# Kernel tuning notes

Measured on AMD Instinct MI355X. Metric: run time of the kernel, lower is better.

Reference implementation:

```python
import jax, jax.numpy as jnp
import numpy as np

SOFT_TAU = 0.5
MAX_TEMP = 40.0
LABEL_SMOOTH = 0.1


def setup_inputs() -> dict:
    key = jax.random.key(0)
    k1, k2 = jax.random.split(key)
    B, Tv, Tw, D = 64, 128, 128, 256
    video_features = jax.random.normal(k1, (B, Tv, D), dtype=jnp.float32)
    wifi_features = jax.random.normal(k2, (B, Tw, D), dtype=jnp.float32)
    logit_scale = jnp.ones((), dtype=jnp.float32)
    return {"video_features": video_features, "wifi_features": wifi_features, "logit_scale": logit_scale}


def _cross_entropy_ls(logits, labels):
    # torch CrossEntropyLoss(label_smoothing=0.1), mean reduction
    logp = jax.nn.log_softmax(logits, axis=-1)
    nll = -jnp.take_along_axis(logp, labels[:, None], axis=1)[:, 0]
    smooth = -jnp.mean(logp, axis=-1)
    return jnp.mean((1.0 - LABEL_SMOOTH) * nll + LABEL_SMOOTH * smooth)


def reference(video_features, wifi_features, logit_scale):
    B = video_features.shape[0]
    # [B, B, Tv, Tw] dense cross-modal similarity
    sim = jnp.einsum('imd,jnd->ijmn', video_features, wifi_features)
    sim_d = jax.lax.stop_gradient(sim)
    # video->wifi soft pooling over Tw
    attn_v2w = jax.nn.softmax(sim_d / SOFT_TAU, axis=3)
    soft_sim_v2w = jnp.sum(sim * attn_v2w, axis=3)  # [B, B, Tv]
    # wifi->video soft pooling over Tv
    attn_w2v = jax.nn.softmax(sim_d / SOFT_TAU, axis=2)
    soft_sim_w2v = jnp.sum(sim * attn_w2v, axis=2)  # [B, B, Tw]
    # frame-level softmax pooling to global similarity
    fw_v = jax.nn.softmax(jax.lax.stop_gradient(soft_sim_v2w) / SOFT_TAU, axis=2)
    sim_v2w_global = jnp.sum(soft_sim_v2w * fw_v, axis=2)  # [B, B]
    fw_w = jax.nn.softmax(jax.lax.stop_gradient(soft_sim_w2v) / SOFT_TAU, axis=2)
    sim_w2v_global = jnp.sum(soft_sim_w2v * fw_w, axis=2)  # [B, B]
    dense_similarity = (sim_v2w_global + sim_w2v_global) / 2.0
    scale = jnp.minimum(logit_scale, MAX_TEMP)
    logits_per_video = scale * dense_similarity
    logits_per_wifi = logits_per_video.T
    labels = jnp.arange(B, dtype=jnp.int32)
    loss_video = _cross_entropy_ls(logits_per_video, labels)
    loss_wifi = _cross_entropy_ls(logits_per_wifi, labels)
    return (loss_video + loss_wifi) / 2.0
```

## Files before the change

kernel.cpp:

```cpp
#include <hip/hip_runtime.h>
#include <hip/hip_bf16.h>

typedef __attribute__((ext_vector_type(8))) short bf16x8;
typedef __attribute__((ext_vector_type(4))) float f32x4;

#define TT 128
#define DD 256
#define BK 64
#define BPAN 16384

__device__ __forceinline__ unsigned short f2bf(float f) {
  unsigned int x = __float_as_uint(f);
  x += 0x7fffu + ((x >> 16) & 1u);
  return (unsigned short)(x >> 16);
}

__device__ __forceinline__ bf16x8 pack8(float4 lo, float4 hi) {
  bf16x8 v;
  v[0] = (short)f2bf(lo.x); v[1] = (short)f2bf(lo.y);
  v[2] = (short)f2bf(lo.z); v[3] = (short)f2bf(lo.w);
  v[4] = (short)f2bf(hi.x); v[5] = (short)f2bf(hi.y);
  v[6] = (short)f2bf(hi.z); v[7] = (short)f2bf(hi.w);
  return v;
}

__global__ __launch_bounds__(512, 4) void pair_kernel(
    const float* __restrict__ video, const float* __restrict__ wifi,
    float* __restrict__ dense) {
  __shared__ __align__(16) char lds[65536];
  const int tid = threadIdx.x;
  const int bid = blockIdx.x;
  const int bi = bid >> 6, bj = bid & 63;
  const float* __restrict__ Ag = video + (size_t)bi * (TT * DD);
  const float* __restrict__ Bg = wifi  + (size_t)bj * (TT * DD);

  const int wid = tid >> 6, l = tid & 63;
  const int l15 = l & 15;
  const int R   = (wid >> 1) * 32;
  const int Cc  = (wid & 1) * 64;
  const int xr  = (l15 & 7) << 4;
  const int lhi16 = (l >> 4) * 16;

  const int srow  = tid >> 2;
  const int scolb = (tid & 3) * 32;
  const int sswz  = (srow & 7) << 4;
  const int sb0 = srow * 128 + ((scolb)      ^ sswz);
  const int sb1 = srow * 128 + ((scolb + 16) ^ sswz);

  f32x4 acc[2][4];
#pragma unroll
  for (int m = 0; m < 2; ++m)
#pragma unroll
    for (int n = 0; n < 4; ++n) acc[m][n] = (f32x4){0.f, 0.f, 0.f, 0.f};

  const int arow0 = (R + l15) * 128;
  const int arow1 = (R + 16 + l15) * 128;
  const int brow0 = (Cc +  0 + l15) * 128 + BPAN;
  const int brow1 = (Cc + 16 + l15) * 128 + BPAN;
  const int brow2 = (Cc + 32 + l15) * 128 + BPAN;
  const int brow3 = (Cc + 48 + l15) * 128 + BPAN;

  for (int kp = 0; kp < 4; ++kp) {
    const float* pa = Ag + srow * DD + kp * BK + (tid & 3) * 16;
    const float* pb = Bg + srow * DD + kp * BK + (tid & 3) * 16;
    float4 a0 = *(const float4*)(pa);
    float4 a1 = *(const float4*)(pa + 4);
    float4 a2 = *(const float4*)(pa + 8);
    float4 a3 = *(const float4*)(pa + 12);
    float4 b0 = *(const float4*)(pb);
    float4 b1 = *(const float4*)(pb + 4);
    float4 b2 = *(const float4*)(pb + 8);
    float4 b3 = *(const float4*)(pb + 12);
    if (kp) __syncthreads();
    *(bf16x8*)(lds + sb0)        = pack8(a0, a1);
    *(bf16x8*)(lds + sb1)        = pack8(a2, a3);
    *(bf16x8*)(lds + BPAN + sb0) = pack8(b0, b1);
    *(bf16x8*)(lds + BPAN + sb1) = pack8(b2, b3);
    __syncthreads();

#pragma unroll
    for (int ks = 0; ks < 2; ++ks) {
      const int ko = (ks * 64 + lhi16) ^ xr;
      bf16x8 fa0 = *(const bf16x8*)(lds + arow0 + ko);
      bf16x8 fa1 = *(const bf16x8*)(lds + arow1 + ko);
      bf16x8 fb0 = *(const bf16x8*)(lds + brow0 + ko);
      bf16x8 fb1 = *(const bf16x8*)(lds + brow1 + ko);
      bf16x8 fb2 = *(const bf16x8*)(lds + brow2 + ko);
      bf16x8 fb3 = *(const bf16x8*)(lds + brow3 + ko);
      acc[0][0] = __builtin_amdgcn_mfma_f32_16x16x32_bf16(fa0, fb0, acc[0][0], 0, 0, 0);
      acc[0][1] = __builtin_amdgcn_mfma_f32_16x16x32_bf16(fa0, fb1, acc[0][1], 0, 0, 0);
      acc[0][2] = __builtin_amdgcn_mfma_f32_16x16x32_bf16(fa0, fb2, acc[0][2], 0, 0, 0);
      acc[0][3] = __builtin_amdgcn_mfma_f32_16x16x32_bf16(fa0, fb3, acc[0][3], 0, 0, 0);
      acc[1][0] = __builtin_amdgcn_mfma_f32_16x16x32_bf16(fa1, fb0, acc[1][0], 0, 0, 0);
      acc[1][1] = __builtin_amdgcn_mfma_f32_16x16x32_bf16(fa1, fb1, acc[1][1], 0, 0, 0);
      acc[1][2] = __builtin_amdgcn_mfma_f32_16x16x32_bf16(fa1, fb2, acc[1][2], 0, 0, 0);
      acc[1][3] = __builtin_amdgcn_mfma_f32_16x16x32_bf16(fa1, fb3, acc[1][3], 0, 0, 0);
    }
  }
  __syncthreads();

  {
    const int rbase = R + (l >> 4) * 4;
    const int cbase = Cc + l15;
#pragma unroll
    for (int m = 0; m < 2; ++m)
#pragma unroll
      for (int n = 0; n < 4; ++n)
#pragma unroll
        for (int reg = 0; reg < 4; ++reg) {
          const int row = rbase + m * 16 + reg;
          const int col = cbase + n * 16;
          *(float*)(lds + row * 512 + ((col * 4) ^ ((row & 7) << 4))) =
              acc[m][n][reg];
        }
  }
  __syncthreads();

  const int r = tid >> 2, g = tid & 3;
  float svv, sww;
  {
    float v[32];
    float mx = -3.4e38f;
    const int rswz = (r & 7) << 4;
#pragma unroll
    for (int c = 0; c < 32; ++c) {
      const int col = g + 4 * c;
      v[c] = *(const float*)(lds + r * 512 + ((col * 4) ^ rswz));
      mx = fmaxf(mx, v[c]);
    }
    mx = fmaxf(mx, __shfl_xor(mx, 1));
    mx = fmaxf(mx, __shfl_xor(mx, 2));
    float se = 0.f, sev = 0.f;
#pragma unroll
    for (int c = 0; c < 32; ++c) {
      float e = __expf((v[c] - mx) * 2.0f);
      se += e; sev += e * v[c];
    }
    se  += __shfl_xor(se, 1);  se  += __shfl_xor(se, 2);
    sev += __shfl_xor(sev, 1); sev += __shfl_xor(sev, 2);
    svv = sev / se;
  }
  {
    float v[32];
    float mx = -3.4e38f;
#pragma unroll
    for (int c = 0; c < 32; ++c) {
      const int row = g + 4 * c;
      v[c] = *(const float*)(lds + row * 512 + ((r * 4) ^ ((row & 7) << 4)));
      mx = fmaxf(mx, v[c]);
    }
    mx = fmaxf(mx, __shfl_xor(mx, 1));
    mx = fmaxf(mx, __shfl_xor(mx, 2));
    float se = 0.f, sev = 0.f;
#pragma unroll
    for (int c = 0; c < 32; ++c) {
      float e = __expf((v[c] - mx) * 2.0f);
      se += e; sev += e * v[c];
    }
    se  += __shfl_xor(se, 1);  se  += __shfl_xor(se, 2);
    sev += __shfl_xor(sev, 1); sev += __shfl_xor(sev, 2);
    sww = sev / se;
  }
  __syncthreads();
  if (g == 0) {
    *(float*)(lds + r * 4)       = svv;
    *(float*)(lds + 512 + r * 4) = sww;
  }
  __syncthreads();

  if (wid < 2) {
    const float* arr = (const float*)(lds + wid * 512);
    float a0 = arr[l], a1 = arr[l + 64];
    float mx = fmaxf(a0, a1);
#pragma unroll
    for (int s = 1; s < 64; s <<= 1) mx = fmaxf(mx, __shfl_xor(mx, s));
    float e0 = __expf((a0 - mx) * 2.0f), e1 = __expf((a1 - mx) * 2.0f);
    float se = e0 + e1, sev = e0 * a0 + e1 * a1;
#pragma unroll
    for (int s = 1; s < 64; s <<= 1) { se += __shfl_xor(se, s); sev += __shfl_xor(sev, s); }
    if (l == 0) *(float*)(lds + 1024 + wid * 4) = sev / se;
  }
  __syncthreads();
  if (tid == 0)
    dense[bid] = 0.5f * (*(const float*)(lds + 1024) + *(const float*)(lds + 1028));
}

__global__ __launch_bounds__(64) void loss_kernel(
    const float* __restrict__ dense, const float* __restrict__ scalep,
    float* __restrict__ out) {
  const int i = threadIdx.x;
  const float sc = fminf(scalep[0], 40.0f);
  float mxr = -3.4e38f, mxc = -3.4e38f;
  for (int j = 0; j < 64; ++j) {
    mxr = fmaxf(mxr, sc * dense[i * 64 + j]);
    mxc = fmaxf(mxc, sc * dense[j * 64 + i]);
  }
  float ser = 0.f, sec = 0.f, slr = 0.f, slc = 0.f;
  for (int j = 0; j < 64; ++j) {
    float zr = sc * dense[i * 64 + j];
    float zc = sc * dense[j * 64 + i];
    ser += __expf(zr - mxr); sec += __expf(zc - mxc);
    slr += zr;               slc += zc;
  }
  const float lser = mxr + logf(ser);
  const float lsec = mxc + logf(sec);
  const float zd = sc * dense[i * 65];
  float lv = lser - 0.9f * zd - 0.1f * (slr * (1.0f / 64.0f));
  float lw = lsec - 0.9f * zd - 0.1f * (slc * (1.0f / 64.0f));
  float t = 0.5f * (lv + lw);
#pragma unroll
  for (int s = 1; s < 64; s <<= 1) t += __shfl_xor(t, s);
  if (i == 0) out[0] = t * (1.0f / 64.0f);
}

extern "C" void kernel_launch(void* const* d_in, const int* in_sizes, int n_in,
                              void* d_out, int out_size, void* d_ws, size_t ws_size,
                              hipStream_t stream) {
  (void)in_sizes; (void)n_in; (void)out_size; (void)ws_size;
  const float* video = (const float*)d_in[0];
  const float* wifi  = (const float*)d_in[1];
  const float* scale = (const float*)d_in[2];
  float* dense = (float*)d_ws;

  hipLaunchKernelGGL(pair_kernel, dim3(64 * 64), dim3(512), 0, stream,
                     video, wifi, dense);
  hipLaunchKernelGGL(loss_kernel, dim3(1), dim3(64), 0, stream,
                     dense, scale, (float*)d_out);
}
```

Baseline: 110.7 us.

## Pre-convert inputs to bf16 and reduce soft-pooling directly from MFMA registers

Adds a conversion kernel that writes bf16 copies of both inputs to workspace once, so each of the 4096 pair blocks loads half the bytes and skips repeated fp32-to-bf16 packing. The epilogue no longer stages the 128x128 similarity tile in LDS. It computes row and column max, exp-sum and weighted sums from accumulator registers with lane shuffles and small partial buffers. LDS drops to 32KB and launch bounds rise to 6 blocks per CU for higher occupancy. The cost is an extra kernel launch and more register pressure, and there is an fp32 fallback when workspace is too small.

```diff
diff --git a/kernel.cpp b/kernel.cpp
--- a/kernel.cpp
+++ b/kernel.cpp
@@ -3,6 +3,7 @@
 
 typedef __attribute__((ext_vector_type(8))) short bf16x8;
 typedef __attribute__((ext_vector_type(4))) float f32x4;
+typedef __attribute__((ext_vector_type(4))) unsigned short u16x4;
 
 #define TT 128
 #define DD 256
@@ -24,15 +25,28 @@
   return v;
 }
 
-__global__ __launch_bounds__(512, 4) void pair_kernel(
-    const float* __restrict__ video, const float* __restrict__ wifi,
+__global__ __launch_bounds__(256) void conv_kernel(
+    const float* __restrict__ v, const float* __restrict__ w,
+    unsigned short* __restrict__ vb, unsigned short* __restrict__ wb) {
+  const int idx = blockIdx.x * 256 + threadIdx.x;
+  float4 a = reinterpret_cast<const float4*>(v)[idx];
+  float4 b = reinterpret_cast<const float4*>(w)[idx];
+  u16x4 pa, pb;
+  pa[0] = f2bf(a.x); pa[1] = f2bf(a.y); pa[2] = f2bf(a.z); pa[3] = f2bf(a.w);
+  pb[0] = f2bf(b.x); pb[1] = f2bf(b.y); pb[2] = f2bf(b.z); pb[3] = f2bf(b.w);
+  reinterpret_cast<u16x4*>(vb)[idx] = pa;
+  reinterpret_cast<u16x4*>(wb)[idx] = pb;
+}
+
+template <bool PRE>
+__global__ __launch_bounds__(512, 6) void pair_kernel(
+    const float* __restrict__ videof, const float* __restrict__ wifif,
+    const unsigned short* __restrict__ videob, const unsigned short* __restrict__ wifib,
     float* __restrict__ dense) {
-  __shared__ __align__(16) char lds[65536];
+  __shared__ __align__(16) char lds[32768];
   const int tid = threadIdx.x;
   const int bid = blockIdx.x;
   const int bi = bid >> 6, bj = bid & 63;
-  const float* __restrict__ Ag = video + (size_t)bi * (TT * DD);
-  const float* __restrict__ Bg = wifi  + (size_t)bj * (TT * DD);
 
   const int wid = tid >> 6, l = tid & 63;
   const int l15 = l & 15;
@@ -61,21 +75,33 @@
   const int brow3 = (Cc + 48 + l15) * 128 + BPAN;
 
   for (int kp = 0; kp < 4; ++kp) {
-    const float* pa = Ag + srow * DD + kp * BK + (tid & 3) * 16;
-    const float* pb = Bg + srow * DD + kp * BK + (tid & 3) * 16;
-    float4 a0 = *(const float4*)(pa);
-    float4 a1 = *(const float4*)(pa + 4);
-    float4 a2 = *(const float4*)(pa + 8);
-    float4 a3 = *(const float4*)(pa + 12);
-    float4 b0 = *(const float4*)(pb);
-    float4 b1 = *(const float4*)(pb + 4);
-    float4 b2 = *(const float4*)(pb + 8);
-    float4 b3 = *(const float4*)(pb + 12);
+    bf16x8 va0, va1, vb0, vb1;
+    if constexpr (PRE) {
+      const unsigned short* pa = videob + (size_t)bi * (TT * DD) + srow * DD + kp * BK + (tid & 3) * 16;
+      const unsigned short* pb = wifib  + (size_t)bj * (TT * DD) + srow * DD + kp * BK + (tid & 3) * 16;
+      va0 = *(const bf16x8*)(pa);
+      va1 = *(const bf16x8*)(pa + 8);
+      vb0 = *(const bf16x8*)(pb);
+      vb1 = *(const bf16x8*)(pb + 8);
+    } else {
+      const float* pa = videof + (size_t)bi * (TT * DD) + srow * DD + kp * BK + (tid & 3) * 16;
+      const float* pb = wifif  + (size_t)bj * (TT * DD) + srow * DD + kp * BK + (tid & 3) * 16;
+      float4 a0 = *(const float4*)(pa);
+      float4 a1 = *(const float4*)(pa + 4);
+      float4 a2 = *(const float4*)(pa + 8);
+      float4 a3 = *(const float4*)(pa + 12);
+      float4 b0 = *(const float4*)(pb);
+      float4 b1 = *(const float4*)(pb + 4);
+      float4 b2 = *(const float4*)(pb + 8);
+      float4 b3 = *(const float4*)(pb + 12);
+      va0 = pack8(a0, a1); va1 = pack8(a2, a3);
+      vb0 = pack8(b0, b1); vb1 = pack8(b2, b3);
+    }
     if (kp) __syncthreads();
-    *(bf16x8*)(lds + sb0)        = pack8(a0, a1);
-    *(bf16x8*)(lds + sb1)        = pack8(a2, a3);
-    *(bf16x8*)(lds + BPAN + sb0) = pack8(b0, b1);
-    *(bf16x8*)(lds + BPAN + sb1) = pack8(b2, b3);
+    *(bf16x8*)(lds + sb0)        = va0;
+    *(bf16x8*)(lds + sb1)        = va1;
+    *(bf16x8*)(lds + BPAN + sb0) = vb0;
+    *(bf16x8*)(lds + BPAN + sb1) = vb1;
     __syncthreads();
 
 #pragma unroll
@@ -99,78 +125,99 @@
   }
   __syncthreads();
 
-  {
-    const int rbase = R + (l >> 4) * 4;
-    const int cbase = Cc + l15;
+  float* F = reinterpret_cast<float*>(lds);
+  float* pmax = F;
+  float* pse  = F + 256;
+  float* psev = F + 512;
+  float* cmax = F + 768;
+  float* cse  = F + 1280;
+  float* csev = F + 1792;
+  float* gbuf = F + 2304;
+
+  const int rbase = R + (l >> 4) * 4;
+
+#pragma unroll
+  for (int m = 0; m < 2; ++m)
+#pragma unroll
+    for (int reg = 0; reg < 4; ++reg) {
+      float mx = fmaxf(fmaxf(acc[m][0][reg], acc[m][1][reg]),
+                       fmaxf(acc[m][2][reg], acc[m][3][reg]));
+      mx = fmaxf(mx, __shfl_xor(mx, 1));
+      mx = fmaxf(mx, __shfl_xor(mx, 2));
+      mx = fmaxf(mx, __shfl_xor(mx, 4));
+      mx = fmaxf(mx, __shfl_xor(mx, 8));
+      if (l15 == 0) pmax[(wid & 1) * 128 + rbase + m * 16 + reg] = mx;
+    }
+#pragma unroll
+  for (int n = 0; n < 4; ++n) {
+    float mx = acc[0][n][0];
+#pragma unroll
+    for (int reg = 1; reg < 4; ++reg) mx = fmaxf(mx, acc[0][n][reg]);
+#pragma unroll
+    for (int reg = 0; reg < 4; ++reg) mx = fmaxf(mx, acc[1][n][reg]);
+    mx = fmaxf(mx, __shfl_xor(mx, 16));
+    mx = fmaxf(mx, __shfl_xor(mx, 32));
+    if (l < 16) cmax[(wid >> 1) * 128 + Cc + n * 16 + l15] = mx;
+  }
+  __syncthreads();
+
+#pragma unroll
+  for (int m = 0; m < 2; ++m)
+#pragma unroll
+    for (int reg = 0; reg < 4; ++reg) {
+      const int row = rbase + m * 16 + reg;
+      const float mx = fmaxf(pmax[row], pmax[128 + row]);
+      float se = 0.f, sev = 0.f;
+#pragma unroll
+      for (int n = 0; n < 4; ++n) {
+        float v = acc[m][n][reg];
+        float e = __expf((v - mx) * 2.0f);
+        se += e; sev += e * v;
+      }
+      se  += __shfl_xor(se, 1);  se  += __shfl_xor(se, 2);
+      se  += __shfl_xor(se, 4);  se  += __shfl_xor(se, 8);
+      sev += __shfl_xor(sev, 1); sev += __shfl_xor(sev, 2);
+      sev += __shfl_xor(sev, 4); sev += __shfl_xor(sev, 8);
+      if (l15 == 0) {
+        pse [(wid & 1) * 128 + row] = se;
+        psev[(wid & 1) * 128 + row] = sev;
+      }
+    }
+#pragma unroll
+  for (int n = 0; n < 4; ++n) {
+    const int col = Cc + n * 16 + l15;
+    const float mx = fmaxf(fmaxf(cmax[col], cmax[128 + col]),
+                           fmaxf(cmax[256 + col], cmax[384 + col]));
+    float se = 0.f, sev = 0.f;
 #pragma unroll
     for (int m = 0; m < 2; ++m)
 #pragma unroll
-      for (int n = 0; n < 4; ++n)
-#pragma unroll
-        for (int reg = 0; reg < 4; ++reg) {
-          const int row = rbase + m * 16 + reg;
-          const int col = cbase + n * 16;
-          *(float*)(lds + row * 512 + ((col * 4) ^ ((row & 7) << 4))) =
-              acc[m][n][reg];
-        }
-  }
-  __syncthreads();
-
-  const int r = tid >> 2, g = tid & 3;
-  float svv, sww;
-  {
-    float v[32];
-    float mx = -3.4e38f;
-    const int rswz = (r & 7) << 4;
-#pragma unroll
-    for (int c = 0; c < 32; ++c) {
-      const int col = g + 4 * c;
-      v[c] = *(const float*)(lds + r * 512 + ((col * 4) ^ rswz));
-      mx = fmaxf(mx, v[c]);
-    }
-    mx = fmaxf(mx, __shfl_xor(mx, 1));
-    mx = fmaxf(mx, __shfl_xor(mx, 2));
-    float se = 0.f, sev = 0.f;
-#pragma unroll
-    for (int c = 0; c < 32; ++c) {
-      float e = __expf((v[c] - mx) * 2.0f);
-      se += e; sev += e * v[c];
-    }
-    se  += __shfl_xor(se, 1);  se  += __shfl_xor(se, 2);
-    sev += __shfl_xor(sev, 1); sev += __shfl_xor(sev, 2);
-    svv = sev / se;
-  }
-  {
-    float v[32];
-    float mx = -3.4e38f;
-#pragma unroll
-    for (int c = 0; c < 32; ++c) {
-      const int row = g + 4 * c;
-      v[c] = *(const float*)(lds + row * 512 + ((r * 4) ^ ((row & 7) << 4)));
-      mx = fmaxf(mx, v[c]);
-    }
-    mx = fmaxf(mx, __shfl_xor(mx, 1));
-    mx = fmaxf(mx, __shfl_xor(mx, 2));
-    float se = 0.f, sev = 0.f;
-#pragma unroll
-    for (int c = 0; c < 32; ++c) {
-      float e = __expf((v[c] - mx) * 2.0f);
-      se += e; sev += e * v[c];
-    }
-    se  += __shfl_xor(se, 1);  se  += __shfl_xor(se, 2);
-    sev += __shfl_xor(sev, 1); sev += __shfl_xor(sev, 2);
-    sww = sev / se;
-  }
-  __syncthreads();
-  if (g == 0) {
-    *(float*)(lds + r * 4)       = svv;
-    *(float*)(lds + 512 + r * 4) = sww;
+      for (int reg = 0; reg < 4; ++reg) {
+        float v = acc[m][n][reg];
+        float e = __expf((v - mx) * 2.0f);
+        se += e; sev += e * v;
+      }
+    se  += __shfl_xor(se, 16);  se  += __shfl_xor(se, 32);
+    sev += __shfl_xor(sev, 16); sev += __shfl_xor(sev, 32);
+    if (l < 16) {
+      cse [(wid >> 1) * 128 + col] = se;
+      csev[(wid >> 1) * 128 + col] = sev;
+    }
   }
   __syncthreads();
 
   if (wid < 2) {
-    const float* arr = (const float*)(lds + wid * 512);
-    float a0 = arr[l], a1 = arr[l + 64];
+    float a0, a1;
+    if (wid == 0) {
+      a0 = (psev[l]      + psev[128 + l])      / (pse[l]      + pse[128 + l]);
+      a1 = (psev[64 + l] + psev[192 + l])      / (pse[64 + l] + pse[192 + l]);
+    } else {
+      float s0 = cse[l] + cse[128 + l] + cse[256 + l] + cse[384 + l];
+      float v0 = csev[l] + csev[128 + l] + csev[256 + l] + csev[384 + l];
+      float s1 = cse[64 + l] + cse[192 + l] + cse[320 + l] + cse[448 + l];
+      float v1 = csev[64 + l] + csev[192 + l] + csev[320 + l] + csev[448 + l];
+      a0 = v0 / s0; a1 = v1 / s1;
+    }
     float mx = fmaxf(a0, a1);
 #pragma unroll
     for (int s = 1; s < 64; s <<= 1) mx = fmaxf(mx, __shfl_xor(mx, s));
@@ -178,11 +225,10 @@
     float se = e0 + e1, sev = e0 * a0 + e1 * a1;
 #pragma unroll
     for (int s = 1; s < 64; s <<= 1) { se += __shfl_xor(se, s); sev += __shfl_xor(sev, s); }
-    if (l == 0) *(float*)(lds + 1024 + wid * 4) = sev / se;
-  }
-  __syncthreads();
-  if (tid == 0)
-    dense[bid] = 0.5f * (*(const float*)(lds + 1024) + *(const float*)(lds + 1028));
+    if (l == 0) gbuf[wid] = sev / se;
+  }
+  __syncthreads();
+  if (tid == 0) dense[bid] = 0.5f * (gbuf[0] + gbuf[1]);
 }
 
 __global__ __launch_bounds__(64) void loss_kernel(
@@ -216,14 +262,24 @@
 extern "C" void kernel_launch(void* const* d_in, const int* in_sizes, int n_in,
                               void* d_out, int out_size, void* d_ws, size_t ws_size,
                               hipStream_t stream) {
-  (void)in_sizes; (void)n_in; (void)out_size; (void)ws_size;
+  (void)in_sizes; (void)n_in; (void)out_size;
   const float* video = (const float*)d_in[0];
   const float* wifi  = (const float*)d_in[1];
   const float* scale = (const float*)d_in[2];
   float* dense = (float*)d_ws;
-
-  hipLaunchKernelGGL(pair_kernel, dim3(64 * 64), dim3(512), 0, stream,
-                     video, wifi, dense);
+  unsigned short* vb = (unsigned short*)((char*)d_ws + 16384);
+  unsigned short* wb = vb + 64 * TT * DD;
+
+  const bool pre = ws_size >= (size_t)16384 + 2u * 64 * TT * DD * 2;
+  if (pre) {
+    hipLaunchKernelGGL(conv_kernel, dim3(2048), dim3(256), 0, stream,
+                       video, wifi, vb, wb);
+    hipLaunchKernelGGL((pair_kernel<true>), dim3(64 * 64), dim3(512), 0, stream,
+                       video, wifi, vb, wb, dense);
+  } else {
+    hipLaunchKernelGGL((pair_kernel<false>), dim3(64 * 64), dim3(512), 0, stream,
+                       video, wifi, vb, wb, dense);
+  }
   hipLaunchKernelGGL(loss_kernel, dim3(1), dim3(64), 0, stream,
                      dense, scale, (float*)d_out);
 }
```

After: 99.99 us. 9.7% less time.
